# Kernel optimization log

Hardware: AMD Instinct MI355X
Metric: run time of the kernel (lower is better)

## Reference

```python
import jax, jax.numpy as jnp
import numpy as np

V = 2_000_000
NNZ = 14_000_000
N_MESHES = 4


def setup_inputs() -> dict:
    key = jax.random.key(0)
    k1, k2, k3, k4, k5, k6 = jax.random.split(key, 6)
    verts = jax.random.normal(k1, (V, 3), dtype=jnp.float32)
    lap_vals = jax.random.normal(k2, (NNZ,), dtype=jnp.float32)
    lap_rows = jax.random.randint(k3, (NNZ,), 0, V, dtype=jnp.int32)
    lap_cols = jax.random.randint(k4, (NNZ,), 0, V, dtype=jnp.int32)
    verts_mesh_idx = jnp.sort(jax.random.randint(k5, (V,), 0, N_MESHES, dtype=jnp.int32))
    coefs = jax.random.uniform(k6, (V,), dtype=jnp.float32)
    return {"verts": verts, "lap_vals": lap_vals, "lap_rows": lap_rows,
            "lap_cols": lap_cols, "verts_mesh_idx": verts_mesh_idx, "coefs": coefs}


def reference(verts, lap_vals, lap_rows, lap_cols, verts_mesh_idx, coefs):
    # Sparse Laplacian (COO) x vertex coords: L.mm(verts_packed)  [V,3]
    Lx = jax.ops.segment_sum(lap_vals[:, None] * verts[lap_cols], lap_rows,
                             num_segments=V)
    # norm_w = 1/rowsum where rowsum > 0, else unchanged (torch.sparse.sum dim=1)
    row_sum = jax.ops.segment_sum(lap_vals, lap_rows, num_segments=V)
    norm_w = jnp.where(row_sum > 0, 1.0 / jnp.where(row_sum > 0, row_sum, 1.0),
                       row_sum)[:, None]
    # 'cot' branch: loss = L.mm(verts) * norm_w - verts, then per-row L2 norm
    res = Lx * norm_w - verts
    loss = jnp.sqrt(jnp.sum(res * res, axis=1))  # [V]
    # weights = 1 / num_verts_per_mesh gathered per packed vertex
    nvpm = jnp.bincount(verts_mesh_idx, length=N_MESHES)
    weights = 1.0 / nvpm[verts_mesh_idx].astype(jnp.float32)
    loss = loss * weights * coefs
    return jnp.sum(loss) / N_MESHES
```

## Files before the change

kernel.cpp:

```cpp
#include <hip/hip_runtime.h>


#define NB 1024
#define BMAX 2048
#define BROWS 2048
#define SEG_SHIFT 17
#define NSEG_MAX 16

typedef unsigned int uintv4 __attribute__((ext_vector_type(4)));
typedef unsigned int uintv2 __attribute__((ext_vector_type(2)));

__global__ void hist_kernel(const int* __restrict__ rows, int nnz, int cpb,
                            int B, unsigned short* __restrict__ hist,
                            const float* __restrict__ verts, int V,
                            float4* __restrict__ verts4) {
    if (verts4) {
        int stride = gridDim.x * blockDim.x;
        for (int vtx = blockIdx.x * blockDim.x + threadIdx.x; vtx < V;
             vtx += stride) {
            verts4[vtx] = make_float4(verts[3 * vtx + 0], verts[3 * vtx + 1],
                                      verts[3 * vtx + 2], 0.f);
        }
    }
    __shared__ unsigned h[BMAX];
    for (int b = threadIdx.x; b < B; b += blockDim.x) h[b] = 0;
    __syncthreads();
    int k = blockIdx.x;
    int i0 = k * cpb;
    int i1 = min(i0 + cpb, nnz);
    for (int i = i0 + 4 * (int)threadIdx.x; i < i1; i += 4 * blockDim.x) {
        if (i + 3 < i1) {
            int4 r4 = *(const int4*)(rows + i);
            atomicAdd(&h[r4.x >> 11], 1u);
            atomicAdd(&h[r4.y >> 11], 1u);
            atomicAdd(&h[r4.z >> 11], 1u);
            atomicAdd(&h[r4.w >> 11], 1u);
        } else {
            for (int j = i; j < i1; ++j) atomicAdd(&h[rows[j] >> 11], 1u);
        }
    }
    __syncthreads();
    for (int b = threadIdx.x; b < B; b += blockDim.x)
        hist[(size_t)b * NB + k] = (unsigned short)h[b];
}

__global__ void scan_blocks_kernel(unsigned short* __restrict__ hist,
                                   unsigned* __restrict__ total) {
    int b = blockIdx.x;
    int t = threadIdx.x;
    int lane = t & 63, wave = t >> 6;
    unsigned short* hp = hist + (size_t)b * NB;
    ushort4 hv = ((const ushort4*)hp)[t];
    unsigned a0 = hv.x, a1 = hv.y, a2 = hv.z, a3 = hv.w;
    unsigned sum = a0 + a1 + a2 + a3;
    unsigned x = sum;
    for (int off = 1; off < 64; off <<= 1) {
        unsigned y = __shfl_up(x, off);
        if (lane >= off) x += y;
    }
    __shared__ unsigned wsum[4];
    if (lane == 63) wsum[wave] = x;
    __syncthreads();
    unsigned woff = 0;
    for (int w = 0; w < wave; ++w) woff += wsum[w];
    unsigned excl = woff + x - sum;
    ushort4 ov;
    ov.x = (unsigned short)excl;
    ov.y = (unsigned short)(excl + a0);
    ov.z = (unsigned short)(excl + a0 + a1);
    ov.w = (unsigned short)(excl + a0 + a1 + a2);
    ((ushort4*)hp)[t] = ov;
    if (t == 255) total[b] = woff + x;
}

__global__ void scan_buckets_kernel(const unsigned* __restrict__ total,
                                    unsigned* __restrict__ base, int B,
                                    const int* __restrict__ mesh_idx, int v,
                                    int* __restrict__ nvpm) {
    int t = threadIdx.x;
    if (t < 4) {
        auto lb = [&](int tgt) {
            int lo = 0, hi = v;
            while (lo < hi) {
                int mid = (lo + hi) >> 1;
                if (mesh_idx[mid] < tgt) lo = mid + 1; else hi = mid;
            }
            return lo;
        };
        nvpm[t] = lb(t + 1) - lb(t);
    }
    __shared__ unsigned buf0[1024], buf1[1024];
    unsigned x0 = (2 * t < B) ? total[2 * t] : 0u;
    unsigned x1 = (2 * t + 1 < B) ? total[2 * t + 1] : 0u;
    unsigned pair = x0 + x1;
    buf0[t] = pair;
    __syncthreads();
    unsigned* src = buf0;
    unsigned* dst = buf1;
    unsigned vv = pair;
    for (int off = 1; off < 1024; off <<= 1) {
        vv = src[t];
        if (t >= off) vv += src[t - off];
        dst[t] = vv;
        __syncthreads();
        unsigned* tmp = src; src = dst; dst = tmp;
    }
    unsigned excl = vv - pair;
    base[2 * t] = excl;
    base[2 * t + 1] = excl + x0;
    if (t == 1023) base[2048] = vv;
}

__global__ void scatter_kernel(const int* __restrict__ rows,
                               const int* __restrict__ cols,
                               const float* __restrict__ vals,
                               const unsigned short* __restrict__ hist,
                               const unsigned* __restrict__ base,
                               uint2* __restrict__ dst,
                               int nnz, int cpb, int B) {
    __shared__ unsigned cur[BMAX];
    int k = blockIdx.x;
    for (int b = threadIdx.x; b < B; b += blockDim.x)
        cur[b] = base[b] + hist[(size_t)b * NB + k];
    __syncthreads();
    int i0 = k * cpb;
    int i1 = min(i0 + cpb, nnz);
    for (int i = i0 + 4 * (int)threadIdx.x; i < i1; i += 4 * blockDim.x) {
        if (i + 3 < i1) {
            int4   r4 = *(const int4*)(rows + i);
            int4   c4 = *(const int4*)(cols + i);
            float4 v4 = *(const float4*)(vals + i);
            unsigned p0 = atomicAdd(&cur[r4.x >> 11], 1u);
            unsigned p1 = atomicAdd(&cur[r4.y >> 11], 1u);
            unsigned p2 = atomicAdd(&cur[r4.z >> 11], 1u);
            unsigned p3 = atomicAdd(&cur[r4.w >> 11], 1u);
            uint2 e0, e1, e2, e3;
            e0.x = ((unsigned)(r4.x & (BROWS - 1)) << 21) | (unsigned)c4.x;
            e0.y = __float_as_uint(v4.x);
            e1.x = ((unsigned)(r4.y & (BROWS - 1)) << 21) | (unsigned)c4.y;
            e1.y = __float_as_uint(v4.y);
            e2.x = ((unsigned)(r4.z & (BROWS - 1)) << 21) | (unsigned)c4.z;
            e2.y = __float_as_uint(v4.z);
            e3.x = ((unsigned)(r4.w & (BROWS - 1)) << 21) | (unsigned)c4.w;
            e3.y = __float_as_uint(v4.w);
            dst[p0] = e0;
            dst[p1] = e1;
            dst[p2] = e2;
            dst[p3] = e3;
        } else {
            for (int j = i; j < i1; ++j) {
                int r = rows[j];
                unsigned p = atomicAdd(&cur[r >> 11], 1u);
                uint2 e;
                e.x = ((unsigned)(r & (BROWS - 1)) << 21) | (unsigned)cols[j];
                e.y = __float_as_uint(vals[j]);
                dst[p] = e;
            }
        }
    }
}

__global__ void resort_kernel(const uint2* __restrict__ src,
                              const unsigned* __restrict__ base,
                              uint2* __restrict__ dst,
                              unsigned* __restrict__ segoff, int nseg) {
    int b = blockIdx.x;
    unsigned s0 = base[b], s1 = base[b + 1];
    __shared__ unsigned cnt[8][NSEG_MAX];
    __shared__ unsigned cur[NSEG_MAX];
    int wave = threadIdx.x >> 6;
    for (int s = threadIdx.x; s < 8 * NSEG_MAX; s += blockDim.x)
        ((unsigned*)cnt)[s] = 0;
    __syncthreads();
    for (unsigned i = s0 + threadIdx.x; i < s1; i += blockDim.x) {
        unsigned ex = ((const unsigned*)(src + i))[0];
        atomicAdd(&cnt[wave][(ex & 0x1FFFFFu) >> SEG_SHIFT], 1u);
    }
    __syncthreads();
    if (threadIdx.x == 0) {
        unsigned acc = s0;
        for (int s = 0; s < nseg; ++s) {
            unsigned c = 0;
            for (int w = 0; w < 8; ++w) c += cnt[w][s];
            cur[s] = acc;
            segoff[b * 17 + s] = acc;
            acc += c;
        }
        segoff[b * 17 + nseg] = acc;
    }
    __syncthreads();
    for (unsigned i = s0 + threadIdx.x; i < s1; i += blockDim.x) {
        uint2 e = src[i];
        unsigned p = atomicAdd(&cur[(e.x & 0x1FFFFFu) >> SEG_SHIFT], 1u);
        dst[p] = e;
    }
}

__global__ void bucket_seg_kernel(const uint2* __restrict__ entries,
                                  const unsigned* __restrict__ segoff,
                                  const float4* __restrict__ verts4,
                                  const float* __restrict__ coefs,
                                  const int* __restrict__ mesh_idx,
                                  const int* __restrict__ nvpm,
                                  double* __restrict__ partial, int V,
                                  int nseg) {
    __shared__ float ax[BROWS], ay[BROWS], az[BROWS], aw[BROWS];
    int b = blockIdx.x;
    for (int j = threadIdx.x; j < BROWS; j += blockDim.x) {
        ax[j] = 0.f; ay[j] = 0.f; az[j] = 0.f; aw[j] = 0.f;
    }
    __syncthreads();
    for (int s = 0; s < nseg; ++s) {
        unsigned r0 = segoff[b * 17 + s];
        unsigned r1 = segoff[b * 17 + s + 1];
        for (unsigned i = r0 + threadIdx.x; i < r1; i += blockDim.x) {
            uintv2 e = __builtin_nontemporal_load((const uintv2*)(entries + i));
            unsigned lr = e.x >> 21;
            unsigned c  = e.x & 0x1FFFFFu;
            float4 p = verts4[c];
            float v = __uint_as_float(e.y);
            atomicAdd(&ax[lr], v * p.x);
            atomicAdd(&ay[lr], v * p.y);
            atomicAdd(&az[lr], v * p.z);
            atomicAdd(&aw[lr], v);
        }
    }
    __syncthreads();

    float inv0 = 1.0f / (float)nvpm[0];
    float inv1 = 1.0f / (float)nvpm[1];
    float inv2 = 1.0f / (float)nvpm[2];
    float inv3 = 1.0f / (float)nvpm[3];

    double acc = 0.0;
    int r0 = b << 11;
    for (int j = threadIdx.x; j < BROWS; j += blockDim.x) {
        int r = r0 + j;
        if (r < V) {
            float rs = aw[j];
            float nw = (rs > 0.0f) ? (1.0f / rs) : rs;
            float4 p = verts4[r];
            float d0 = ax[j] * nw - p.x;
            float d1 = ay[j] * nw - p.y;
            float d2 = az[j] * nw - p.z;
            float loss = sqrtf(d0 * d0 + d1 * d1 + d2 * d2);
            int m = __builtin_nontemporal_load(mesh_idx + r);
            float w = (m == 0) ? inv0 : (m == 1) ? inv1 : (m == 2) ? inv2 : inv3;
            acc += (double)(loss * w * __builtin_nontemporal_load(coefs + r));
        }
    }

    __shared__ double sred[512];
    sred[threadIdx.x] = acc;
    __syncthreads();
    for (int s = blockDim.x / 2; s > 0; s >>= 1) {
        if (threadIdx.x < s) sred[threadIdx.x] += sred[threadIdx.x + s];
        __syncthreads();
    }
    if (threadIdx.x == 0) atomicAdd(partial, sred[0]);
}

template <bool V4>
__global__ void bucket_kernel(const uint2* __restrict__ entries,
                              const unsigned* __restrict__ base,
                              const float* __restrict__ verts,
                              const float4* __restrict__ verts4,
                              const float* __restrict__ coefs,
                              const int* __restrict__ mesh_idx,
                              const int* __restrict__ nvpm,
                              double* __restrict__ partial, int V) {
    __shared__ float ax[BROWS], ay[BROWS], az[BROWS], aw[BROWS];
    int b = blockIdx.x;
    for (int j = threadIdx.x; j < BROWS; j += blockDim.x) {
        ax[j] = 0.f; ay[j] = 0.f; az[j] = 0.f; aw[j] = 0.f;
    }
    __syncthreads();
    unsigned s0 = base[b], s1 = base[b + 1];

    auto gather3 = [&](unsigned c, float& x, float& y, float& z) {
        if (V4) {
            float4 p = verts4[c];
            x = p.x; y = p.y; z = p.z;
        } else {
            x = verts[3 * c + 0];
            y = verts[3 * c + 1];
            z = verts[3 * c + 2];
        }
    };
    auto atomics = [&](unsigned ex, unsigned ey, float x, float y, float z) {
        unsigned lr = ex >> 21;
        float v = __uint_as_float(ey);
        atomicAdd(&ax[lr], v * x);
        atomicAdd(&ay[lr], v * y);
        atomicAdd(&az[lr], v * z);
        atomicAdd(&aw[lr], v);
    };

    for (unsigned i = s0 + threadIdx.x; i < s1; i += blockDim.x) {
        uint2 e = entries[i];
        float x, y, z;
        gather3(e.x & 0x1FFFFFu, x, y, z);
        atomics(e.x, e.y, x, y, z);
    }
    __syncthreads();

    float inv0 = 1.0f / (float)nvpm[0];
    float inv1 = 1.0f / (float)nvpm[1];
    float inv2 = 1.0f / (float)nvpm[2];
    float inv3 = 1.0f / (float)nvpm[3];

    double acc = 0.0;
    int r0 = b << 11;
    for (int j = threadIdx.x; j < BROWS; j += blockDim.x) {
        int r = r0 + j;
        if (r < V) {
            float rs = aw[j];
            float nw = (rs > 0.0f) ? (1.0f / rs) : rs;
            float vx, vy, vz;
            gather3((unsigned)r, vx, vy, vz);
            float d0 = ax[j] * nw - vx;
            float d1 = ay[j] * nw - vy;
            float d2 = az[j] * nw - vz;
            float loss = sqrtf(d0 * d0 + d1 * d1 + d2 * d2);
            int m = mesh_idx[r];
            float w = (m == 0) ? inv0 : (m == 1) ? inv1 : (m == 2) ? inv2 : inv3;
            acc += (double)(loss * w * coefs[r]);
        }
    }

    __shared__ double sred[512];
    sred[threadIdx.x] = acc;
    __syncthreads();
    for (int s = blockDim.x / 2; s > 0; s >>= 1) {
        if (threadIdx.x < s) sred[threadIdx.x] += sred[threadIdx.x + s];
        __syncthreads();
    }
    if (threadIdx.x == 0) atomicAdd(partial, sred[0]);
}

__global__ void write_out_kernel(const double* __restrict__ partial,
                                 float* __restrict__ out) {
    if (threadIdx.x == 0 && blockIdx.x == 0)
        out[0] = (float)(partial[0] * 0.25);
}


__global__ void fb_mesh_counts_kernel(const int* __restrict__ mesh_idx, int v,
                                      int* __restrict__ nvpm) {
    int m = threadIdx.x;
    if (m >= 4) return;
    auto lb = [&](int t) {
        int lo = 0, hi = v;
        while (lo < hi) {
            int mid = (lo + hi) >> 1;
            if (mesh_idx[mid] < t) lo = mid + 1; else hi = mid;
        }
        return lo;
    };
    nvpm[m] = lb(m + 1) - lb(m);
}

__global__ void fb_scatter_kernel(const float* __restrict__ verts,
                                  const float* __restrict__ vals,
                                  const int* __restrict__ rows,
                                  const int* __restrict__ cols,
                                  float* __restrict__ acc, int nnz) {
    int i = blockIdx.x * blockDim.x + threadIdx.x;
    if (i >= nnz) return;
    int r = rows[i];
    int c = cols[i];
    float v = vals[i];
    float* p = acc + 4ll * r;
    atomicAdd(p + 0, v * verts[3 * c + 0]);
    atomicAdd(p + 1, v * verts[3 * c + 1]);
    atomicAdd(p + 2, v * verts[3 * c + 2]);
    atomicAdd(p + 3, v);
}

__global__ void fb_finalize_kernel(const float* __restrict__ verts,
                                   const float* __restrict__ coefs,
                                   const int* __restrict__ mesh_idx,
                                   const float4* __restrict__ acc,
                                   const int* __restrict__ nvpm,
                                   double* __restrict__ partial, int v) {
    float inv0 = 1.0f / (float)nvpm[0];
    float inv1 = 1.0f / (float)nvpm[1];
    float inv2 = 1.0f / (float)nvpm[2];
    float inv3 = 1.0f / (float)nvpm[3];
    double acc_sum = 0.0;
    for (int i = blockIdx.x * blockDim.x + threadIdx.x; i < v;
         i += gridDim.x * blockDim.x) {
        float4 a = acc[i];
        float rs = a.w;
        float nw = (rs > 0.0f) ? (1.0f / rs) : rs;
        float r0 = a.x * nw - verts[3 * i + 0];
        float r1 = a.y * nw - verts[3 * i + 1];
        float r2 = a.z * nw - verts[3 * i + 2];
        float loss = sqrtf(r0 * r0 + r1 * r1 + r2 * r2);
        int m = mesh_idx[i];
        float w = (m == 0) ? inv0 : (m == 1) ? inv1 : (m == 2) ? inv2 : inv3;
        acc_sum += (double)(loss * w * coefs[i]);
    }
    __shared__ double sred[256];
    sred[threadIdx.x] = acc_sum;
    __syncthreads();
    for (int s = blockDim.x / 2; s > 0; s >>= 1) {
        if (threadIdx.x < s) sred[threadIdx.x] += sred[threadIdx.x + s];
        __syncthreads();
    }
    if (threadIdx.x == 0) atomicAdd(partial, sred[0]);
}

extern "C" void kernel_launch(void* const* d_in, const int* in_sizes, int n_in,
                              void* d_out, int out_size, void* d_ws, size_t ws_size,
                              hipStream_t stream) {
    const float* verts    = (const float*)d_in[0];
    const float* lap_vals = (const float*)d_in[1];
    const int*   lap_rows = (const int*)d_in[2];
    const int*   lap_cols = (const int*)d_in[3];
    const int*   mesh_idx = (const int*)d_in[4];
    const float* coefs    = (const float*)d_in[5];
    float* out = (float*)d_out;

    const int V   = in_sizes[0] / 3;
    const int NNZ = in_sizes[1];
    const int B   = (V + BROWS - 1) / BROWS;
    const int nseg = (V + (1 << SEG_SHIFT) - 1) >> SEG_SHIFT;
    int cpb = (NNZ + NB - 1) / NB;
    cpb = (cpb + 3) & ~3;

    char* ws = (char*)d_ws;
    const size_t off_hist     = 262144;
    const size_t off_entries  = off_hist + (size_t)BMAX * NB * 2;
    const size_t off_entries2 = off_entries + (size_t)NNZ * 8;
    double*         partial  = (double*)(ws + 0);
    int*            nvpm     = (int*)(ws + 8);
    unsigned*       base     = (unsigned*)(ws + 64);
    unsigned*       total    = (unsigned*)(ws + 16384);
    unsigned*       segoff   = (unsigned*)(ws + 32768);
    unsigned short* hist     = (unsigned short*)(ws + off_hist);
    uint2*          entries  = (uint2*)(ws + off_entries);
    uint2*          entries2 = (uint2*)(ws + off_entries2);

    size_t sort_need = off_entries2 + 64;
    size_t v4_need   = off_entries2 + (size_t)16 * V + 64;
    size_t seg_need  = off_entries2 + (size_t)NNZ * 8 + (size_t)16 * V + 64;

    (void)hipMemsetAsync(d_ws, 0, 64, stream);

    if (ws_size >= sort_need && B <= BMAX && V <= (1 << 21)) {
        bool seg = (ws_size >= seg_need) && (nseg <= NSEG_MAX);
        bool v4  = seg || (ws_size >= v4_need);
        float4* verts4 = seg ? (float4*)(ws + off_entries2 + (size_t)NNZ * 8)
                             : (float4*)(ws + off_entries2);
        hist_kernel<<<NB, 256, 0, stream>>>(lap_rows, NNZ, cpb, B, hist,
                                            verts, V, v4 ? verts4 : nullptr);
        scan_blocks_kernel<<<B, 256, 0, stream>>>(hist, total);
        scan_buckets_kernel<<<1, 1024, 0, stream>>>(total, base, B,
                                                    mesh_idx, V, nvpm);
        scatter_kernel<<<NB, 256, 0, stream>>>(lap_rows, lap_cols, lap_vals,
                                               hist, base, entries, NNZ, cpb, B);
        if (seg) {
            resort_kernel<<<B, 512, 0, stream>>>(entries, base, entries2,
                                                 segoff, nseg);
            bucket_seg_kernel<<<B, 512, 0, stream>>>(entries2, segoff, verts4,
                                                     coefs, mesh_idx, nvpm,
                                                     partial, V, nseg);
        } else if (v4) {
            bucket_kernel<true><<<B, 512, 0, stream>>>(
                entries, base, verts, verts4, coefs, mesh_idx, nvpm, partial, V);
        } else {
            bucket_kernel<false><<<B, 512, 0, stream>>>(
                entries, base, verts, verts4, coefs, mesh_idx, nvpm, partial, V);
        }
    } else {
        float* acc = (float*)(ws + 64);
        (void)hipMemsetAsync(ws + 64, 0, (size_t)16 * V, stream);
        fb_mesh_counts_kernel<<<1, 64, 0, stream>>>(mesh_idx, V, nvpm);
        fb_scatter_kernel<<<(NNZ + 255) / 256, 256, 0, stream>>>(
            verts, lap_vals, lap_rows, lap_cols, acc, NNZ);
        fb_finalize_kernel<<<2048, 256, 0, stream>>>(
            verts, coefs, mesh_idx, (const float4*)acc, nvpm, partial, V);
    }

    write_out_kernel<<<1, 64, 0, stream>>>(partial, out);
}
```

Measured before the change: 755.7 us.

## Add soft grid barrier between column segments and derive mesh weights from boundaries

Adds a spin-wait grid-wide barrier (with a spin limit) after each column segment in bucket_seg_kernel. All blocks then gather from the same range of verts4 at roughly the same time, which should keep that range resident in L2. It also stores the mesh boundary indices from scan_buckets_kernel, so the finalize loop picks per-row weights by comparison instead of loading mesh_idx. The barrier adds idle time and depends on all blocks being co-resident, which the added launch bounds aim to allow; the spin cap keeps it from deadlocking.

```diff
diff --git a/kernel.cpp b/kernel.cpp
--- a/kernel.cpp
+++ b/kernel.cpp
@@ -76,7 +76,8 @@
 __global__ void scan_buckets_kernel(const unsigned* __restrict__ total,
                                     unsigned* __restrict__ base, int B,
                                     const int* __restrict__ mesh_idx, int v,
-                                    int* __restrict__ nvpm) {
+                                    int* __restrict__ nvpm,
+                                    int* __restrict__ bnd) {
     int t = threadIdx.x;
     if (t < 4) {
         auto lb = [&](int tgt) {
@@ -87,7 +88,9 @@
             }
             return lo;
         };
-        nvpm[t] = lb(t + 1) - lb(t);
+        int hi_b = lb(t + 1);
+        nvpm[t] = hi_b - lb(t);
+        bnd[t]  = hi_b;
     }
     __shared__ unsigned buf0[1024], buf1[1024];
     unsigned x0 = (2 * t < B) ? total[2 * t] : 0u;
@@ -196,14 +199,16 @@
     }
 }
 
-__global__ void bucket_seg_kernel(const uint2* __restrict__ entries,
-                                  const unsigned* __restrict__ segoff,
-                                  const float4* __restrict__ verts4,
-                                  const float* __restrict__ coefs,
-                                  const int* __restrict__ mesh_idx,
-                                  const int* __restrict__ nvpm,
-                                  double* __restrict__ partial, int V,
-                                  int nseg) {
+__global__ void __launch_bounds__(512, 8)
+bucket_seg_kernel(const uint2* __restrict__ entries,
+                  const unsigned* __restrict__ segoff,
+                  const float4* __restrict__ verts4,
+                  const float* __restrict__ coefs,
+                  const int* __restrict__ bnd,
+                  const int* __restrict__ nvpm,
+                  unsigned* __restrict__ arrive,
+                  double* __restrict__ partial, int V,
+                  int nseg, int nblocks) {
     __shared__ float ax[BROWS], ay[BROWS], az[BROWS], aw[BROWS];
     int b = blockIdx.x;
     for (int j = threadIdx.x; j < BROWS; j += blockDim.x) {
@@ -224,6 +229,22 @@
             atomicAdd(&az[lr], v * p.z);
             atomicAdd(&aw[lr], v);
         }
+        if (nblocks > 0 && s + 1 < nseg) {
+            __syncthreads();
+            if (threadIdx.x == 0) {
+                __hip_atomic_fetch_add(&arrive[s], 1u, __ATOMIC_RELAXED,
+                                       __HIP_MEMORY_SCOPE_AGENT);
+                int spins = 0;
+                while (__hip_atomic_load(&arrive[s], __ATOMIC_RELAXED,
+                                         __HIP_MEMORY_SCOPE_AGENT)
+                           < (unsigned)nblocks &&
+                       spins < 2000) {
+                    __builtin_amdgcn_s_sleep(2);
+                    ++spins;
+                }
+            }
+            __syncthreads();
+        }
     }
     __syncthreads();
 
@@ -231,6 +252,7 @@
     float inv1 = 1.0f / (float)nvpm[1];
     float inv2 = 1.0f / (float)nvpm[2];
     float inv3 = 1.0f / (float)nvpm[3];
+    int bd0 = bnd[0], bd1 = bnd[1], bd2 = bnd[2];
 
     double acc = 0.0;
     int r0 = b << 11;
@@ -244,8 +266,8 @@
             float d1 = ay[j] * nw - p.y;
             float d2 = az[j] * nw - p.z;
             float loss = sqrtf(d0 * d0 + d1 * d1 + d2 * d2);
-            int m = __builtin_nontemporal_load(mesh_idx + r);
-            float w = (m == 0) ? inv0 : (m == 1) ? inv1 : (m == 2) ? inv2 : inv3;
+            float w = (r < bd0) ? inv0 : (r < bd1) ? inv1 : (r < bd2) ? inv2
+                                                                      : inv3;
             acc += (double)(loss * w * __builtin_nontemporal_load(coefs + r));
         }
     }
@@ -435,8 +457,10 @@
     const size_t off_entries2 = off_entries + (size_t)NNZ * 8;
     double*         partial  = (double*)(ws + 0);
     int*            nvpm     = (int*)(ws + 8);
+    int*            bnd      = (int*)(ws + 24);
     unsigned*       base     = (unsigned*)(ws + 64);
     unsigned*       total    = (unsigned*)(ws + 16384);
+    unsigned*       arrive   = (unsigned*)(ws + 24576);
     unsigned*       segoff   = (unsigned*)(ws + 32768);
     unsigned short* hist     = (unsigned short*)(ws + off_hist);
     uint2*          entries  = (uint2*)(ws + off_entries);
@@ -447,6 +471,7 @@
     size_t seg_need  = off_entries2 + (size_t)NNZ * 8 + (size_t)16 * V + 64;
 
     (void)hipMemsetAsync(d_ws, 0, 64, stream);
+    (void)hipMemsetAsync(ws + 24576, 0, 64, stream);
 
     if (ws_size >= sort_need && B <= BMAX && V <= (1 << 21)) {
         bool seg = (ws_size >= seg_need) && (nseg <= NSEG_MAX);
@@ -457,15 +482,17 @@
                                             verts, V, v4 ? verts4 : nullptr);
         scan_blocks_kernel<<<B, 256, 0, stream>>>(hist, total);
         scan_buckets_kernel<<<1, 1024, 0, stream>>>(total, base, B,
-                                                    mesh_idx, V, nvpm);
+                                                    mesh_idx, V, nvpm, bnd);
         scatter_kernel<<<NB, 256, 0, stream>>>(lap_rows, lap_cols, lap_vals,
                                                hist, base, entries, NNZ, cpb, B);
         if (seg) {
             resort_kernel<<<B, 512, 0, stream>>>(entries, base, entries2,
                                                  segoff, nseg);
+            int nblocks_bar = (B <= 1024) ? B : 0;
             bucket_seg_kernel<<<B, 512, 0, stream>>>(entries2, segoff, verts4,
-                                                     coefs, mesh_idx, nvpm,
-                                                     partial, V, nseg);
+                                                     coefs, bnd, nvpm, arrive,
+                                                     partial, V, nseg,
+                                                     nblocks_bar);
         } else if (v4) {
             bucket_kernel<true><<<B, 512, 0, stream>>>(
                 entries, base, verts, verts4, coefs, mesh_idx, nvpm, partial, V);
```

Measured after the change: 1.484 ms. 96.3% more time.

## Fuse resort and accumulate into per-row counting sort with register accumulation

Applied to the files above, without the earlier changes.

Replaces the two-kernel path (segment resort by column range, then shared-memory atomic accumulation) with one kernel. That kernel counting-sorts each bucket's entries by local row, then has each thread walk its rows' entries and sum them in registers. Per-entry LDS float atomics go away, one launch goes away, and mesh weights now come from precomputed boundaries instead of reading mesh_idx. The trade-off is losing the column-segment locality of the vertex gathers. Threads also face imbalanced serial per-row loops, and each row's entries are read back right after the scatter in the same kernel.

```diff
diff --git a/kernel.cpp b/kernel.cpp
--- a/kernel.cpp
+++ b/kernel.cpp
@@ -4,10 +4,7 @@
 #define NB 1024
 #define BMAX 2048
 #define BROWS 2048
-#define SEG_SHIFT 17
-#define NSEG_MAX 16
-
-typedef unsigned int uintv4 __attribute__((ext_vector_type(4)));
+
 typedef unsigned int uintv2 __attribute__((ext_vector_type(2)));
 
 __global__ void hist_kernel(const int* __restrict__ rows, int nnz, int cpb,
@@ -76,7 +73,8 @@
 __global__ void scan_buckets_kernel(const unsigned* __restrict__ total,
                                     unsigned* __restrict__ base, int B,
                                     const int* __restrict__ mesh_idx, int v,
-                                    int* __restrict__ nvpm) {
+                                    int* __restrict__ nvpm,
+                                    int* __restrict__ bnd) {
     int t = threadIdx.x;
     if (t < 4) {
         auto lb = [&](int tgt) {
@@ -87,7 +85,9 @@
             }
             return lo;
         };
-        nvpm[t] = lb(t + 1) - lb(t);
+        int hi_b = lb(t + 1);
+        nvpm[t] = hi_b - lb(t);
+        bnd[t]  = hi_b;
     }
     __shared__ unsigned buf0[1024], buf1[1024];
     unsigned x0 = (2 * t < B) ? total[2 * t] : 0u;
@@ -160,70 +160,54 @@
     }
 }
 
-__global__ void resort_kernel(const uint2* __restrict__ src,
-                              const unsigned* __restrict__ base,
-                              uint2* __restrict__ dst,
-                              unsigned* __restrict__ segoff, int nseg) {
+__global__ void __launch_bounds__(512)
+rowsort_accum_kernel(const uint2* __restrict__ entries,
+                     const unsigned* __restrict__ base,
+                     uint2* __restrict__ entries2,
+                     const float4* __restrict__ verts4,
+                     const float* __restrict__ coefs,
+                     const int* __restrict__ bnd,
+                     const int* __restrict__ nvpm,
+                     double* __restrict__ partial, int V) {
+    __shared__ unsigned cnt[BROWS];
+    __shared__ unsigned rp[BROWS];
+    __shared__ unsigned cur[BROWS];
+    __shared__ unsigned wsum[8];
+    __shared__ double sred[512];
     int b = blockIdx.x;
+    int t = threadIdx.x;
     unsigned s0 = base[b], s1 = base[b + 1];
-    __shared__ unsigned cnt[8][NSEG_MAX];
-    __shared__ unsigned cur[NSEG_MAX];
-    int wave = threadIdx.x >> 6;
-    for (int s = threadIdx.x; s < 8 * NSEG_MAX; s += blockDim.x)
-        ((unsigned*)cnt)[s] = 0;
-    __syncthreads();
-    for (unsigned i = s0 + threadIdx.x; i < s1; i += blockDim.x) {
-        unsigned ex = ((const unsigned*)(src + i))[0];
-        atomicAdd(&cnt[wave][(ex & 0x1FFFFFu) >> SEG_SHIFT], 1u);
-    }
-    __syncthreads();
-    if (threadIdx.x == 0) {
-        unsigned acc = s0;
-        for (int s = 0; s < nseg; ++s) {
-            unsigned c = 0;
-            for (int w = 0; w < 8; ++w) c += cnt[w][s];
-            cur[s] = acc;
-            segoff[b * 17 + s] = acc;
-            acc += c;
-        }
-        segoff[b * 17 + nseg] = acc;
-    }
-    __syncthreads();
-    for (unsigned i = s0 + threadIdx.x; i < s1; i += blockDim.x) {
-        uint2 e = src[i];
-        unsigned p = atomicAdd(&cur[(e.x & 0x1FFFFFu) >> SEG_SHIFT], 1u);
-        dst[p] = e;
-    }
-}
-
-__global__ void bucket_seg_kernel(const uint2* __restrict__ entries,
-                                  const unsigned* __restrict__ segoff,
-                                  const float4* __restrict__ verts4,
-                                  const float* __restrict__ coefs,
-                                  const int* __restrict__ mesh_idx,
-                                  const int* __restrict__ nvpm,
-                                  double* __restrict__ partial, int V,
-                                  int nseg) {
-    __shared__ float ax[BROWS], ay[BROWS], az[BROWS], aw[BROWS];
-    int b = blockIdx.x;
-    for (int j = threadIdx.x; j < BROWS; j += blockDim.x) {
-        ax[j] = 0.f; ay[j] = 0.f; az[j] = 0.f; aw[j] = 0.f;
-    }
-    __syncthreads();
-    for (int s = 0; s < nseg; ++s) {
-        unsigned r0 = segoff[b * 17 + s];
-        unsigned r1 = segoff[b * 17 + s + 1];
-        for (unsigned i = r0 + threadIdx.x; i < r1; i += blockDim.x) {
-            uintv2 e = __builtin_nontemporal_load((const uintv2*)(entries + i));
-            unsigned lr = e.x >> 21;
-            unsigned c  = e.x & 0x1FFFFFu;
-            float4 p = verts4[c];
-            float v = __uint_as_float(e.y);
-            atomicAdd(&ax[lr], v * p.x);
-            atomicAdd(&ay[lr], v * p.y);
-            atomicAdd(&az[lr], v * p.z);
-            atomicAdd(&aw[lr], v);
-        }
+
+    for (int j = t; j < BROWS; j += 512) cnt[j] = 0;
+    __syncthreads();
+    for (unsigned i = s0 + t; i < s1; i += 512) {
+        unsigned ex = ((const unsigned*)(entries + i))[0];
+        atomicAdd(&cnt[ex >> 21], 1u);
+    }
+    __syncthreads();
+    unsigned a0 = cnt[4 * t + 0], a1 = cnt[4 * t + 1];
+    unsigned a2 = cnt[4 * t + 2], a3 = cnt[4 * t + 3];
+    unsigned s = a0 + a1 + a2 + a3;
+    int lane = t & 63, wave = t >> 6;
+    unsigned x = s;
+    for (int off = 1; off < 64; off <<= 1) {
+        unsigned y = __shfl_up(x, off);
+        if (lane >= off) x += y;
+    }
+    if (lane == 63) wsum[wave] = x;
+    __syncthreads();
+    unsigned woff = 0;
+    for (int w = 0; w < wave; ++w) woff += wsum[w];
+    unsigned excl = s0 + woff + x - s;
+    rp[4 * t + 0] = excl;              cur[4 * t + 0] = excl;
+    rp[4 * t + 1] = excl + a0;         cur[4 * t + 1] = excl + a0;
+    rp[4 * t + 2] = excl + a0 + a1;    cur[4 * t + 2] = excl + a0 + a1;
+    rp[4 * t + 3] = excl + a0 + a1 + a2; cur[4 * t + 3] = excl + a0 + a1 + a2;
+    __syncthreads();
+    for (unsigned i = s0 + t; i < s1; i += 512) {
+        uint2 e = entries[i];
+        unsigned p = atomicAdd(&cur[e.x >> 21], 1u);
+        entries2[p] = e;
     }
     __syncthreads();
 
@@ -231,33 +215,42 @@
     float inv1 = 1.0f / (float)nvpm[1];
     float inv2 = 1.0f / (float)nvpm[2];
     float inv3 = 1.0f / (float)nvpm[3];
+    int bd0 = bnd[0], bd1 = bnd[1], bd2 = bnd[2];
 
     double acc = 0.0;
     int r0 = b << 11;
-    for (int j = threadIdx.x; j < BROWS; j += blockDim.x) {
+    #pragma unroll
+    for (int q = 0; q < 4; ++q) {
+        int j = 4 * t + q;
         int r = r0 + j;
         if (r < V) {
-            float rs = aw[j];
-            float nw = (rs > 0.0f) ? (1.0f / rs) : rs;
-            float4 p = verts4[r];
-            float d0 = ax[j] * nw - p.x;
-            float d1 = ay[j] * nw - p.y;
-            float d2 = az[j] * nw - p.z;
+            float sx = 0.f, sy = 0.f, sz = 0.f, sw = 0.f;
+            unsigned e0 = rp[j], e1 = cur[j];
+            for (unsigned k = e0; k < e1; ++k) {
+                uintv2 e = *(const uintv2*)(entries2 + k);
+                float4 p = verts4[e.x & 0x1FFFFFu];
+                float v = __uint_as_float(e.y);
+                sx += v * p.x; sy += v * p.y; sz += v * p.z; sw += v;
+            }
+            float nw = (sw > 0.0f) ? (1.0f / sw) : sw;
+            float4 pv = verts4[r];
+            float d0 = sx * nw - pv.x;
+            float d1 = sy * nw - pv.y;
+            float d2 = sz * nw - pv.z;
             float loss = sqrtf(d0 * d0 + d1 * d1 + d2 * d2);
-            int m = __builtin_nontemporal_load(mesh_idx + r);
-            float w = (m == 0) ? inv0 : (m == 1) ? inv1 : (m == 2) ? inv2 : inv3;
-            acc += (double)(loss * w * __builtin_nontemporal_load(coefs + r));
-        }
-    }
-
-    __shared__ double sred[512];
-    sred[threadIdx.x] = acc;
-    __syncthreads();
-    for (int s = blockDim.x / 2; s > 0; s >>= 1) {
-        if (threadIdx.x < s) sred[threadIdx.x] += sred[threadIdx.x + s];
+            float w = (r < bd0) ? inv0 : (r < bd1) ? inv1 : (r < bd2) ? inv2
+                                                                      : inv3;
+            acc += (double)(loss * w * coefs[r]);
+        }
+    }
+
+    sred[t] = acc;
+    __syncthreads();
+    for (int st = 256; st > 0; st >>= 1) {
+        if (t < st) sred[t] += sred[t + st];
         __syncthreads();
     }
-    if (threadIdx.x == 0) atomicAdd(partial, sred[0]);
+    if (t == 0) atomicAdd(partial, sred[0]);
 }
 
 template <bool V4>
@@ -425,7 +418,6 @@
     const int V   = in_sizes[0] / 3;
     const int NNZ = in_sizes[1];
     const int B   = (V + BROWS - 1) / BROWS;
-    const int nseg = (V + (1 << SEG_SHIFT) - 1) >> SEG_SHIFT;
     int cpb = (NNZ + NB - 1) / NB;
     cpb = (cpb + 3) & ~3;
 
@@ -435,37 +427,35 @@
     const size_t off_entries2 = off_entries + (size_t)NNZ * 8;
     double*         partial  = (double*)(ws + 0);
     int*            nvpm     = (int*)(ws + 8);
+    int*            bnd      = (int*)(ws + 24);
     unsigned*       base     = (unsigned*)(ws + 64);
     unsigned*       total    = (unsigned*)(ws + 16384);
-    unsigned*       segoff   = (unsigned*)(ws + 32768);
     unsigned short* hist     = (unsigned short*)(ws + off_hist);
     uint2*          entries  = (uint2*)(ws + off_entries);
     uint2*          entries2 = (uint2*)(ws + off_entries2);
 
     size_t sort_need = off_entries2 + 64;
     size_t v4_need   = off_entries2 + (size_t)16 * V + 64;
-    size_t seg_need  = off_entries2 + (size_t)NNZ * 8 + (size_t)16 * V + 64;
+    size_t rs_need   = off_entries2 + (size_t)NNZ * 8 + (size_t)16 * V + 64;
 
     (void)hipMemsetAsync(d_ws, 0, 64, stream);
 
     if (ws_size >= sort_need && B <= BMAX && V <= (1 << 21)) {
-        bool seg = (ws_size >= seg_need) && (nseg <= NSEG_MAX);
-        bool v4  = seg || (ws_size >= v4_need);
-        float4* verts4 = seg ? (float4*)(ws + off_entries2 + (size_t)NNZ * 8)
-                             : (float4*)(ws + off_entries2);
+        bool rs  = (ws_size >= rs_need);
+        bool v4  = rs || (ws_size >= v4_need);
+        float4* verts4 = rs ? (float4*)(ws + off_entries2 + (size_t)NNZ * 8)
+                            : (float4*)(ws + off_entries2);
         hist_kernel<<<NB, 256, 0, stream>>>(lap_rows, NNZ, cpb, B, hist,
                                             verts, V, v4 ? verts4 : nullptr);
         scan_blocks_kernel<<<B, 256, 0, stream>>>(hist, total);
         scan_buckets_kernel<<<1, 1024, 0, stream>>>(total, base, B,
-                                                    mesh_idx, V, nvpm);
+                                                    mesh_idx, V, nvpm, bnd);
         scatter_kernel<<<NB, 256, 0, stream>>>(lap_rows, lap_cols, lap_vals,
                                                hist, base, entries, NNZ, cpb, B);
-        if (seg) {
-            resort_kernel<<<B, 512, 0, stream>>>(entries, base, entries2,
-                                                 segoff, nseg);
-            bucket_seg_kernel<<<B, 512, 0, stream>>>(entries2, segoff, verts4,
-                                                     coefs, mesh_idx, nvpm,
-                                                     partial, V, nseg);
+        if (rs) {
+            rowsort_accum_kernel<<<B, 512, 0, stream>>>(entries, base, entries2,
+                                                        verts4, coefs, bnd,
+                                                        nvpm, partial, V);
         } else if (v4) {
             bucket_kernel<true><<<B, 512, 0, stream>>>(
                 entries, base, verts, verts4, coefs, mesh_idx, nvpm, partial, V);
```

Result: slower. 1.043 ms (+38.0%).
